# Kernel tuning notes

Measured on AMD Instinct MI355X. Metric: run time of the kernel, lower is better.

The kernel has to match this reference:

```python
import jax, jax.numpy as jnp
import numpy as np
from math import factorial as _f

# ---------- Wigner 3j / real Clebsch-Gordan (numpy, build-time) ----------

def _w3j(j1, j2, j3, m1, m2, m3):
    if m1 + m2 + m3 != 0 or not (abs(j1 - j2) <= j3 <= j1 + j2):
        return 0.0
    t1, t2 = j2 - m1 - j3, j1 + m2 - j3
    t3, t4, t5 = j1 + j2 - j3, j1 - m1, j2 + m2
    s = 0.0
    for t in range(max(0, t1, t2), min(t3, t4, t5) + 1):
        s += (-1.0) ** t / (_f(t) * _f(t - t1) * _f(t - t2) * _f(t3 - t) * _f(t4 - t) * _f(t5 - t))
    n = ((-1.0) ** (j1 - j2 - m3)
         * (_f(j1 + j2 - j3) * _f(j1 - j2 + j3) * _f(-j1 + j2 + j3) / _f(j1 + j2 + j3 + 1)) ** 0.5
         * (_f(j1 + m1) * _f(j1 - m1) * _f(j2 + m2) * _f(j2 - m2) * _f(j3 + m3) * _f(j3 - m3)) ** 0.5)
    return n * s


def _Umat(l):
    # complex -> real spherical-harmonic basis change
    U = np.zeros((2 * l + 1, 2 * l + 1), dtype=complex)
    U[l, l] = 1.0
    s2 = 1.0 / np.sqrt(2.0)
    for m in range(1, l + 1):
        U[l + m, l + m] = (-1.0) ** m * s2
        U[l + m, l - m] = s2
        U[l - m, l - m] = 1j * s2
        U[l - m, l + m] = -1j * (-1.0) ** m * s2
    return U


def _real_cg(l1, l2, l3):
    Cc = np.zeros((2 * l1 + 1, 2 * l2 + 1, 2 * l3 + 1), dtype=complex)
    for m1 in range(-l1, l1 + 1):
        for m2 in range(-l2, l2 + 1):
            m3 = m1 + m2
            if abs(m3) <= l3:
                Cc[l1 + m1, l2 + m2, l3 + m3] = ((-1.0) ** (l1 - l2 + m3) * np.sqrt(2 * l3 + 1)
                                                 * _w3j(l1, l2, l3, m1, m2, -m3))
    C = np.einsum('am,bn,co,mno->abc', _Umat(l1), _Umat(l2), np.conj(_Umat(l3)), Cc)
    C = C.imag if np.abs(C.imag).sum() > np.abs(C.real).sum() else C.real
    C = C / np.sqrt((C ** 2).sum())  # w3j normalization
    return (C * np.sqrt(2 * l3 + 1)).astype(np.float32)  # component normalization

_TRIPLES = [(1, 1, 2), (1, 2, 3), (0, 0, 0), (1, 1, 0), (2, 2, 0),
            (0, 1, 1), (1, 0, 1), (1, 2, 1), (2, 1, 1), (3, 2, 1),
            (0, 2, 2), (2, 0, 2), (2, 2, 2), (3, 1, 2)]
_CG = {k: jnp.asarray(_real_cg(*k)) for k in _TRIPLES}

# tensor-product channel lists: (l_Y, l_V) pairs producing each output l (filter 0e+1o+2e)
_P_L0 = [(0, 0), (1, 1), (2, 2)]
_P_L1 = [(0, 1), (1, 0), (1, 2), (2, 1), (3, 2)]
_P_L2 = [(0, 2), (1, 1), (2, 0), (2, 2), (3, 1)]
_EPS = 0.1       # epsilon (~1/sqrt(avg_num_neighbors))
_ENV_P = 6       # polynomial envelope order


def _sph(u):
    # component-normalized real spherical harmonics l=0..3 of unit vectors u, m=-l..l order
    E = u.shape[0]
    y0 = jnp.ones((E, 1), u.dtype)
    y1 = np.float32(np.sqrt(3.0)) * u[:, jnp.array([1, 2, 0])]  # real l=1 basis (y,z,x)
    t2 = jnp.einsum('abc,ea,eb->ec', _CG[(1, 1, 2)], y1, y1)
    y2 = t2 * (np.float32(np.sqrt(5.0)) / jnp.linalg.norm(t2, axis=-1, keepdims=True))
    t3 = jnp.einsum('abc,ea,eb->ec', _CG[(1, 2, 3)], y1, y2)
    y3 = t3 * (np.float32(np.sqrt(7.0)) / jnp.linalg.norm(t3, axis=-1, keepdims=True))
    return jnp.concatenate([y0, y1, y2, y3], axis=-1)  # (E,16)


def _lin(h, W):
    return h @ (W / np.float32(np.sqrt(W.shape[0])))  # fan-in normalized linear


def _envelope(d):
    p = _ENV_P
    c1 = np.float32((p + 1) * (p + 2) / 2.0)
    c2 = np.float32(p * (p + 2))
    c3 = np.float32(p * (p + 1) / 2.0)
    f = 1.0 - c1 * d ** p + c2 * d ** (p + 1) - c3 * d ** (p + 2)
    return jnp.where(d < 1.0, f, 0.0)


def _forward(vectors, x, V, senders, n_nodes, W1, W2a, W2b, W2c, Wv1, Wv2):
    E = vectors.shape[0]
    lengths = jnp.linalg.norm(vectors, axis=-1)            # (E,)
    Y = _sph(vectors / lengths[:, None])                   # (E,16)
    w = _lin(x, W1)                                        # (E,64) edge weights
    wY = w[:, :, None] * Y[:, None, :]                     # (E,64,16)
    node = jax.ops.segment_sum(wY, senders, num_segments=n_nodes)
    wY = node[senders] * np.float32(_EPS)                  # scatter_sum with map_back
    A = {0: wY[..., 0:1], 1: wY[..., 1:4], 2: wY[..., 4:9], 3: wY[..., 9:16]}
    B = {0: V[..., 0:1], 1: V[..., 1:4], 2: V[..., 4:9]}

    def tp(pairs, l3):
        outs = [jnp.einsum('abc,eua,eub->euc', _CG[(l1, l2, l3)], A[l1], B[l2])
                for (l1, l2) in pairs]
        return jnp.stack(outs, axis=2)                     # (E,64,n_pairs,2l3+1)

    S = tp(_P_L0, 0).reshape(E, -1)                        # (E,192) 0e scalars -> join x
    V1 = tp(_P_L1, 1).reshape(E, -1, 3)                    # (E,320,3) 1o
    V2 = tp(_P_L2, 2).reshape(E, -1, 5)                    # (E,320,5) 2e

    x2 = jnp.concatenate([x, S], axis=1)                   # (E, d_x+192)
    h = jax.nn.silu(_lin(x2, W2a))
    h = jax.nn.silu(_lin(h, W2b))
    h = _lin(h, W2c)                                       # (E,64), no output act
    x_out = _envelope(lengths)[:, None] * h                # smoothing envelope

    V1o = jnp.einsum('euc,uk->ekc', V1, Wv1 / np.float32(np.sqrt(Wv1.shape[0])))  # (E,64,3)
    V2e = jnp.einsum('euc,uk->ekc', V2, Wv2 / np.float32(np.sqrt(Wv2.shape[0])))  # (E,64,5)
    V_out = jnp.concatenate([V1o.reshape(E, -1), V2e.reshape(E, -1)], axis=1)     # (E,512)
    return x_out, V_out


def setup_inputs() -> dict:
    key = jax.random.key(0)
    ks = jax.random.split(key, 12)
    E, N, DX, MUL = 32768, 2048, 128, 64
    vectors = jax.random.uniform(ks[0], (E, 3), jnp.float32) - 0.5  # |r| < 1 (inside cutoff)
    x = jax.random.normal(ks[1], (E, DX), jnp.float32)
    V = jax.random.normal(ks[2], (E, MUL, 9), jnp.float32)          # 64 slots x (0e+1o+2e)
    senders = jax.random.randint(ks[3], (E,), 0, N)
    species = jax.random.randint(ks[4], (N,), 0, 4, jnp.int32)
    W1 = jax.random.normal(ks[5], (DX, MUL), jnp.float32)
    W2a = jax.random.normal(ks[6], (DX + 192, 64), jnp.float32)
    W2b = jax.random.normal(ks[7], (64, 64), jnp.float32)
    W2c = jax.random.normal(ks[8], (64, 64), jnp.float32)
    Wv1 = jax.random.normal(ks[9], (320, 64), jnp.float32)
    Wv2 = jax.random.normal(ks[10], (320, 64), jnp.float32)
    return dict(vectors=vectors, x=x, V=V, senders=senders, species=species,
                W1=W1, W2a=W2a, W2b=W2b, W2c=W2c, Wv1=Wv1, Wv2=Wv2)


def reference(vectors, x, V, senders, species, W1, W2a, W2b, W2c, Wv1, Wv2):
    # species is unused by the layer body (matches original signature)
    return _forward(vectors, x, V, senders, int(species.shape[0]), W1, W2a, W2b, W2c, Wv1, Wv2)
```

## Files before the change

kernel.cpp:

```cpp
#include <hip/hip_runtime.h>
#include <cmath>
#include <complex>
#include <vector>
#include <algorithm>

namespace {

static double factd(int n) { double r = 1; for (int i = 2; i <= n; i++) r *= i; return r; }
static double par(int k) { return (k % 2 == 0) ? 1.0 : -1.0; }

static double w3j(int j1, int j2, int j3, int m1, int m2, int m3) {
    if (m1 + m2 + m3 != 0) return 0.0;
    if (j3 < std::abs(j1 - j2) || j3 > j1 + j2) return 0.0;
    int t1 = j2 - m1 - j3, t2 = j1 + m2 - j3;
    int t3 = j1 + j2 - j3, t4 = j1 - m1, t5 = j2 + m2;
    int lo = std::max(0, std::max(t1, t2)), hi = std::min(t3, std::min(t4, t5));
    double s = 0.0;
    for (int t = lo; t <= hi; t++)
        s += par(t) / (factd(t) * factd(t - t1) * factd(t - t2) *
                       factd(t3 - t) * factd(t4 - t) * factd(t5 - t));
    double n = par(j1 - j2 - m3)
        * std::sqrt(factd(j1 + j2 - j3) * factd(j1 - j2 + j3) * factd(-j1 + j2 + j3) / factd(j1 + j2 + j3 + 1))
        * std::sqrt(factd(j1 + m1) * factd(j1 - m1) * factd(j2 + m2) * factd(j2 - m2) * factd(j3 + m3) * factd(j3 - m3));
    return n * s;
}

static void Umat(int l, std::complex<double>* U) {
    int n = 2 * l + 1;
    for (int i = 0; i < n * n; i++) U[i] = 0.0;
    U[l * n + l] = 1.0;
    double s2 = 1.0 / std::sqrt(2.0);
    for (int m = 1; m <= l; m++) {
        U[(l + m) * n + (l + m)] = par(m) * s2;
        U[(l + m) * n + (l - m)] = s2;
        U[(l - m) * n + (l - m)] = std::complex<double>(0.0, s2);
        U[(l - m) * n + (l + m)] = std::complex<double>(0.0, -par(m) * s2);
    }
}

static void real_cg(int l1, int l2, int l3, float* out) {
    int n1 = 2 * l1 + 1, n2 = 2 * l2 + 1, n3 = 2 * l3 + 1;
    std::vector<std::complex<double>> Cc((size_t)n1 * n2 * n3, 0.0);
    for (int m1 = -l1; m1 <= l1; m1++)
        for (int m2 = -l2; m2 <= l2; m2++) {
            int m3 = m1 + m2;
            if (std::abs(m3) <= l3)
                Cc[((size_t)(l1 + m1) * n2 + (l2 + m2)) * n3 + (l3 + m3)] =
                    par(l1 - l2 + m3) * std::sqrt((double)(2 * l3 + 1)) * w3j(l1, l2, l3, m1, m2, -m3);
        }
    std::vector<std::complex<double>> U1((size_t)n1 * n1), U2((size_t)n2 * n2), U3((size_t)n3 * n3);
    Umat(l1, U1.data()); Umat(l2, U2.data()); Umat(l3, U3.data());
    std::vector<std::complex<double>> C((size_t)n1 * n2 * n3, 0.0);
    for (int a = 0; a < n1; a++)
        for (int b = 0; b < n2; b++)
            for (int c = 0; c < n3; c++) {
                std::complex<double> s = 0.0;
                for (int m = 0; m < n1; m++)
                    for (int nn = 0; nn < n2; nn++) {
                        std::complex<double> u12 = U1[(size_t)a * n1 + m] * U2[(size_t)b * n2 + nn];
                        if (u12 == std::complex<double>(0.0, 0.0)) continue;
                        for (int o = 0; o < n3; o++) {
                            std::complex<double> cc = Cc[((size_t)m * n2 + nn) * n3 + o];
                            if (cc == std::complex<double>(0.0, 0.0)) continue;
                            s += u12 * std::conj(U3[(size_t)c * n3 + o]) * cc;
                        }
                    }
                C[((size_t)a * n2 + b) * n3 + c] = s;
            }
    double sim = 0, sre = 0;
    for (auto& z : C) { sim += std::abs(z.imag()); sre += std::abs(z.real()); }
    std::vector<double> R(C.size());
    for (size_t i = 0; i < C.size(); i++) R[i] = (sim > sre) ? C[i].imag() : C[i].real();
    double ss = 0; for (double v : R) ss += v * v;
    double scale = std::sqrt((double)(2 * l3 + 1)) / std::sqrt(ss);
    for (size_t i = 0; i < R.size(); i++) out[i] = (float)(R[i] * scale);
}

}

struct CGPack {
    float c000[1];  float c110[9];   float c220[25];
    float c011[9];  float c101[9];   float c121[45];  float c211[45]; float c321[105];
    float c022[25]; float c202[25];  float c222[125]; float c312[105];
    float c112[45]; float c123[105];
};

static void build_pack(CGPack& p) {
    real_cg(0, 0, 0, p.c000); real_cg(1, 1, 0, p.c110); real_cg(2, 2, 0, p.c220);
    real_cg(0, 1, 1, p.c011); real_cg(1, 0, 1, p.c101); real_cg(1, 2, 1, p.c121);
    real_cg(2, 1, 1, p.c211); real_cg(3, 2, 1, p.c321);
    real_cg(0, 2, 2, p.c022); real_cg(2, 0, 2, p.c202); real_cg(2, 2, 2, p.c222);
    real_cg(3, 1, 2, p.c312); real_cg(1, 1, 2, p.c112); real_cg(1, 2, 3, p.c123);
}


template <int NA, int NB, int NC>
__device__ __forceinline__ void tpc(const float* __restrict__ C,
                                    const float* __restrict__ a,
                                    const float* __restrict__ b,
                                    float* __restrict__ out) {
#pragma unroll
    for (int c = 0; c < NC; c++) {
        float s = 0.f;
#pragma unroll
        for (int i = 0; i < NA; i++) {
#pragma unroll
            for (int j = 0; j < NB; j++)
                s += C[(i * NB + j) * NC + c] * a[i] * b[j];
        }
        out[c] = s;
    }
}

template <int NA, int NB, int NC, int ST>
__device__ __forceinline__ void tpcs(const float* __restrict__ C,
                                     const float* __restrict__ a,
                                     const float* __restrict__ b,
                                     float* __restrict__ out) {
#pragma unroll
    for (int c = 0; c < NC; c++) {
        float s = 0.f;
#pragma unroll
        for (int i = 0; i < NA; i++) {
#pragma unroll
            for (int j = 0; j < NB; j++)
                s += C[(i * NB + j) * NC + c] * a[i] * b[j];
        }
        out[c * ST] = s;
    }
}

__device__ __forceinline__ float silu(float v) { return v / (1.f + expf(-v)); }

#define EPSC 0.1f
#define INV_SQRT128 0.08838834764831845f
#define INV_SQRT320 0.05590169943749474f
#define SQRT5 2.2360679774997896f
#define SQRT7 2.6457513110645907f
#define SQRT3 1.7320508075688772f

__global__ __launch_bounds__(256) void k_fuse_wv(
    const float* __restrict__ Wv1, const float* __restrict__ Wv2,
    float2* __restrict__ WvI) {
    int i = blockIdx.x * blockDim.x + threadIdx.x;
    if (i < 320 * 64) WvI[i] = make_float2(Wv1[i], Wv2[i]);
}

__global__ __launch_bounds__(256) void k_edge_pre(
    const float* __restrict__ vectors, const float* __restrict__ x,
    const int* __restrict__ senders, const float* __restrict__ W1,
    float* __restrict__ node, int E, CGPack cg) {
    int wid = (blockIdx.x * blockDim.x + threadIdx.x) >> 6;
    int lane = threadIdx.x & 63;
    if (wid >= E) return;
    int e = wid;
    float vx = vectors[e * 3 + 0], vy = vectors[e * 3 + 1], vz = vectors[e * 3 + 2];
    float inv = rsqrtf(vx * vx + vy * vy + vz * vz);
    float ux = vx * inv, uy = vy * inv, uz = vz * inv;

    float Y[16];
    Y[0] = 1.f;
    float y1[3] = { SQRT3 * uy, SQRT3 * uz, SQRT3 * ux };
    float t2[5]; tpc<3, 3, 5>(cg.c112, y1, y1, t2);
    float n2 = 0.f;
#pragma unroll
    for (int c = 0; c < 5; c++) n2 += t2[c] * t2[c];
    float sc2 = SQRT5 * rsqrtf(n2);
    float y2[5];
#pragma unroll
    for (int c = 0; c < 5; c++) y2[c] = t2[c] * sc2;
    float t3[7]; tpc<3, 5, 7>(cg.c123, y1, y2, t3);
    float n3 = 0.f;
#pragma unroll
    for (int c = 0; c < 7; c++) n3 += t3[c] * t3[c];
    float sc3 = SQRT7 * rsqrtf(n3);
#pragma unroll
    for (int j = 0; j < 3; j++) Y[1 + j] = y1[j];
#pragma unroll
    for (int j = 0; j < 5; j++) Y[4 + j] = y2[j];
#pragma unroll
    for (int j = 0; j < 7; j++) Y[9 + j] = t3[j] * sc3;

    const float* xr = x + (size_t)e * 128;
    float w = 0.f;
#pragma unroll 4
    for (int d = 0; d < 128; d++) w += xr[d] * W1[d * 64 + lane];
    w *= INV_SQRT128;

    int s = senders[e];
    float* nb = node + (size_t)s * 1024 + lane;
#pragma unroll
    for (int k = 0; k < 16; k++) atomicAdd(nb + k * 64, w * Y[k]);
}

__global__ __launch_bounds__(64, 4) void k_edge_main(
    const float* __restrict__ vectors, const float* __restrict__ x,
    const float* __restrict__ V, const int* __restrict__ senders,
    const float* __restrict__ node, const float2* __restrict__ WvI,
    const float* __restrict__ W2a, const float* __restrict__ W2b, const float* __restrict__ W2c,
    float* __restrict__ xout, float* __restrict__ vout, int E, CGPack cg) {
    __shared__ __align__(16) float V1sh[3][320];
    __shared__ __align__(16) float V2sh[5][320];
    __shared__ float Ssh[192];
    __shared__ float Hsh[64];

    int e = blockIdx.x;
    int u = threadIdx.x;
    int s = senders[e];

    const float* nb = node + (size_t)s * 1024 + u;
    float a0 = nb[0] * EPSC;
    float a1[3], a2[5], a3[7];
#pragma unroll
    for (int j = 0; j < 3; j++) a1[j] = nb[(1 + j) * 64] * EPSC;
#pragma unroll
    for (int j = 0; j < 5; j++) a2[j] = nb[(4 + j) * 64] * EPSC;
#pragma unroll
    for (int j = 0; j < 7; j++) a3[j] = nb[(9 + j) * 64] * EPSC;

    const float* vb = V + (size_t)e * 576 + u * 9;
    float b0 = vb[0];
    float b1[3] = { vb[1], vb[2], vb[3] };
    float b2[5] = { vb[4], vb[5], vb[6], vb[7], vb[8] };

    {
        float o[1];
        Ssh[u * 3 + 0] = cg.c000[0] * a0 * b0;
        tpc<3, 3, 1>(cg.c110, a1, b1, o); Ssh[u * 3 + 1] = o[0];
        tpc<5, 5, 1>(cg.c220, a2, b2, o); Ssh[u * 3 + 2] = o[0];
    }
    {
        float* v1 = &V1sh[0][u * 5];
        tpcs<1, 3, 3, 320>(cg.c011, &a0, b1, v1 + 0);
        tpcs<3, 1, 3, 320>(cg.c101, a1, &b0, v1 + 1);
        tpcs<3, 5, 3, 320>(cg.c121, a1, b2, v1 + 2);
        tpcs<5, 3, 3, 320>(cg.c211, a2, b1, v1 + 3);
        tpcs<7, 5, 3, 320>(cg.c321, a3, b2, v1 + 4);
    }
    {
        float* v2 = &V2sh[0][u * 5];
        tpcs<1, 5, 5, 320>(cg.c022, &a0, b2, v2 + 0);
        tpcs<3, 3, 5, 320>(cg.c112, a1, b1, v2 + 1);
        tpcs<5, 1, 5, 320>(cg.c202, a2, &b0, v2 + 2);
        tpcs<5, 5, 5, 320>(cg.c222, a2, b2, v2 + 3);
        tpcs<7, 3, 5, 320>(cg.c312, a3, b1, v2 + 4);
    }
    __syncthreads();

    const float* xr = x + (size_t)e * 128;
    float h = 0.f;
    for (int d = 0; d < 128; d++) h += xr[d] * W2a[d * 64 + u];
    for (int j = 0; j < 192; j++) h += Ssh[j] * W2a[(128 + j) * 64 + u];
    h = silu(h * INV_SQRT320);
    Hsh[u] = h;
    __syncthreads();
    float h2 = 0.f;
    for (int j = 0; j < 64; j++) h2 += Hsh[j] * W2b[j * 64 + u];
    h2 = silu(h2 * 0.125f);
    __syncthreads();
    Hsh[u] = h2;
    __syncthreads();
    float h3 = 0.f;
    for (int j = 0; j < 64; j++) h3 += Hsh[j] * W2c[j * 64 + u];
    h3 *= 0.125f;

    float vx = vectors[e * 3 + 0], vy = vectors[e * 3 + 1], vz = vectors[e * 3 + 2];
    float len = sqrtf(vx * vx + vy * vy + vz * vz);
    float d2 = len * len, d4 = d2 * d2, d6 = d4 * d2, d7 = d6 * len, d8 = d7 * len;
    float env = 1.f - 28.f * d6 + 48.f * d7 - 21.f * d8;
    if (!(len < 1.f)) env = 0.f;
    xout[(size_t)e * 64 + u] = env * h3;

    float acc1[3] = { 0.f, 0.f, 0.f };
    float acc2[5] = { 0.f, 0.f, 0.f, 0.f, 0.f };
    const float2* wvp = WvI + u;
    for (int t4 = 0; t4 < 80; ++t4) {
        int t = t4 * 4;
        float2 w0 = wvp[(t + 0) * 64];
        float2 w1 = wvp[(t + 1) * 64];
        float2 w2 = wvp[(t + 2) * 64];
        float2 w3 = wvp[(t + 3) * 64];
#pragma unroll
        for (int c = 0; c < 3; c++) {
            float4 v = *(const float4*)&V1sh[c][t];
            acc1[c] += v.x * w0.x + v.y * w1.x + v.z * w2.x + v.w * w3.x;
        }
#pragma unroll
        for (int c = 0; c < 5; c++) {
            float4 v = *(const float4*)&V2sh[c][t];
            acc2[c] += v.x * w0.y + v.y * w1.y + v.z * w2.y + v.w * w3.y;
        }
    }
    float* vo = vout + (size_t)e * 512;
#pragma unroll
    for (int c = 0; c < 3; c++) vo[u * 3 + c] = acc1[c] * INV_SQRT320;
#pragma unroll
    for (int c = 0; c < 5; c++) vo[192 + u * 5 + c] = acc2[c] * INV_SQRT320;
}

extern "C" void kernel_launch(void* const* d_in, const int* in_sizes, int n_in,
                              void* d_out, int out_size, void* d_ws, size_t ws_size,
                              hipStream_t stream) {
    const float* vectors = (const float*)d_in[0];
    const float* x       = (const float*)d_in[1];
    const float* V       = (const float*)d_in[2];
    const int*   senders = (const int*)d_in[3];
    const float* W1  = (const float*)d_in[5];
    const float* W2a = (const float*)d_in[6];
    const float* W2b = (const float*)d_in[7];
    const float* W2c = (const float*)d_in[8];
    const float* Wv1 = (const float*)d_in[9];
    const float* Wv2 = (const float*)d_in[10];

    int E = in_sizes[0] / 3;
    int N = in_sizes[4];

    CGPack pack;
    build_pack(pack);

    float*  node = (float*)d_ws;
    float2* WvI  = (float2*)((char*)d_ws + (size_t)N * 1024 * sizeof(float));
    hipMemsetAsync(node, 0, (size_t)N * 1024 * sizeof(float), stream);

    hipLaunchKernelGGL(k_fuse_wv, dim3((320 * 64 + 255) / 256), dim3(256), 0, stream,
                       Wv1, Wv2, WvI);

    dim3 blkA(256), grdA((unsigned)(((size_t)E * 64 + 255) / 256));
    hipLaunchKernelGGL(k_edge_pre, grdA, blkA, 0, stream,
                       vectors, x, senders, W1, node, E, pack);

    float* xout = (float*)d_out;
    float* vout = xout + (size_t)E * 64;
    hipLaunchKernelGGL(k_edge_main, dim3((unsigned)E), dim3(64), 0, stream,
                       vectors, x, V, senders, node, WvI,
                       W2a, W2b, W2c, xout, vout, E, pack);
}
```

Baseline: 747.9 us.

## Repack weights into float4 interleaved layout and make node features lane-contiguous

```diff
diff --git a/kernel.cpp b/kernel.cpp
--- a/kernel.cpp
+++ b/kernel.cpp
@@ -131,6 +131,9 @@
 }
 
 __device__ __forceinline__ float silu(float v) { return v / (1.f + expf(-v)); }
+__device__ __forceinline__ float dot4(float4 a, float4 b) {
+    return a.x * b.x + a.y * b.y + a.z * b.z + a.w * b.w;
+}
 
 #define EPSC 0.1f
 #define INV_SQRT128 0.08838834764831845f
@@ -139,16 +142,45 @@
 #define SQRT7 2.6457513110645907f
 #define SQRT3 1.7320508075688772f
 
-__global__ __launch_bounds__(256) void k_fuse_wv(
+#define N_WVQ  (160 * 64)
+#define N_W2A  (80 * 64)
+#define N_W2B  (16 * 64)
+#define N_W2C  (16 * 64)
+#define N_W1I  (32 * 64)
+
+__global__ __launch_bounds__(256) void k_pack(
     const float* __restrict__ Wv1, const float* __restrict__ Wv2,
-    float2* __restrict__ WvI) {
+    const float* __restrict__ W2a, const float* __restrict__ W2b, const float* __restrict__ W2c,
+    const float* __restrict__ W1,
+    float4* __restrict__ WvQ, float4* __restrict__ W2aI,
+    float4* __restrict__ W2bI, float4* __restrict__ W2cI, float4* __restrict__ W1I) {
     int i = blockIdx.x * blockDim.x + threadIdx.x;
-    if (i < 320 * 64) WvI[i] = make_float2(Wv1[i], Wv2[i]);
+    if (i < N_WVQ) {
+        int t2 = i >> 6, u = i & 63;
+        WvQ[i] = make_float4(Wv1[(2 * t2) * 64 + u], Wv2[(2 * t2) * 64 + u],
+                             Wv1[(2 * t2 + 1) * 64 + u], Wv2[(2 * t2 + 1) * 64 + u]);
+    } else if (i < N_WVQ + N_W2A) {
+        int j = i - N_WVQ; int g = j >> 6, u = j & 63;
+        W2aI[j] = make_float4(W2a[(4 * g) * 64 + u], W2a[(4 * g + 1) * 64 + u],
+                              W2a[(4 * g + 2) * 64 + u], W2a[(4 * g + 3) * 64 + u]);
+    } else if (i < N_WVQ + N_W2A + N_W2B) {
+        int j = i - N_WVQ - N_W2A; int g = j >> 6, u = j & 63;
+        W2bI[j] = make_float4(W2b[(4 * g) * 64 + u], W2b[(4 * g + 1) * 64 + u],
+                              W2b[(4 * g + 2) * 64 + u], W2b[(4 * g + 3) * 64 + u]);
+    } else if (i < N_WVQ + N_W2A + N_W2B + N_W2C) {
+        int j = i - N_WVQ - N_W2A - N_W2B; int g = j >> 6, u = j & 63;
+        W2cI[j] = make_float4(W2c[(4 * g) * 64 + u], W2c[(4 * g + 1) * 64 + u],
+                              W2c[(4 * g + 2) * 64 + u], W2c[(4 * g + 3) * 64 + u]);
+    } else if (i < N_WVQ + N_W2A + N_W2B + N_W2C + N_W1I) {
+        int j = i - N_WVQ - N_W2A - N_W2B - N_W2C; int g = j >> 6, u = j & 63;
+        W1I[j] = make_float4(W1[(4 * g) * 64 + u], W1[(4 * g + 1) * 64 + u],
+                             W1[(4 * g + 2) * 64 + u], W1[(4 * g + 3) * 64 + u]);
+    }
 }
 
 __global__ __launch_bounds__(256) void k_edge_pre(
     const float* __restrict__ vectors, const float* __restrict__ x,
-    const int* __restrict__ senders, const float* __restrict__ W1,
+    const int* __restrict__ senders, const float4* __restrict__ W1I,
     float* __restrict__ node, int E, CGPack cg) {
     int wid = (blockIdx.x * blockDim.x + threadIdx.x) >> 6;
     int lane = threadIdx.x & 63;
@@ -181,42 +213,40 @@
 #pragma unroll
     for (int j = 0; j < 7; j++) Y[9 + j] = t3[j] * sc3;
 
-    const float* xr = x + (size_t)e * 128;
+    const float4* xr4 = (const float4*)(x + (size_t)e * 128);
     float w = 0.f;
-#pragma unroll 4
-    for (int d = 0; d < 128; d++) w += xr[d] * W1[d * 64 + lane];
+#pragma unroll 8
+    for (int g = 0; g < 32; g++) w += dot4(xr4[g], W1I[g * 64 + lane]);
     w *= INV_SQRT128;
 
     int s = senders[e];
-    float* nb = node + (size_t)s * 1024 + lane;
-#pragma unroll
-    for (int k = 0; k < 16; k++) atomicAdd(nb + k * 64, w * Y[k]);
+    float* nb = node + (size_t)s * 1024 + lane * 16;
+#pragma unroll
+    for (int k = 0; k < 16; k++) atomicAdd(nb + k, w * Y[k]);
 }
 
 __global__ __launch_bounds__(64, 4) void k_edge_main(
     const float* __restrict__ vectors, const float* __restrict__ x,
     const float* __restrict__ V, const int* __restrict__ senders,
-    const float* __restrict__ node, const float2* __restrict__ WvI,
-    const float* __restrict__ W2a, const float* __restrict__ W2b, const float* __restrict__ W2c,
+    const float* __restrict__ node, const float4* __restrict__ WvQ,
+    const float4* __restrict__ W2aI, const float4* __restrict__ W2bI, const float4* __restrict__ W2cI,
     float* __restrict__ xout, float* __restrict__ vout, int E, CGPack cg) {
     __shared__ __align__(16) float V1sh[3][320];
     __shared__ __align__(16) float V2sh[5][320];
-    __shared__ float Ssh[192];
-    __shared__ float Hsh[64];
+    __shared__ __align__(16) float Ssh[192];
+    __shared__ __align__(16) float Hsh[64];
 
     int e = blockIdx.x;
     int u = threadIdx.x;
     int s = senders[e];
 
-    const float* nb = node + (size_t)s * 1024 + u;
-    float a0 = nb[0] * EPSC;
-    float a1[3], a2[5], a3[7];
-#pragma unroll
-    for (int j = 0; j < 3; j++) a1[j] = nb[(1 + j) * 64] * EPSC;
-#pragma unroll
-    for (int j = 0; j < 5; j++) a2[j] = nb[(4 + j) * 64] * EPSC;
-#pragma unroll
-    for (int j = 0; j < 7; j++) a3[j] = nb[(9 + j) * 64] * EPSC;
+    const float4* nb4 = (const float4*)(node + (size_t)s * 1024 + u * 16);
+    float4 g0 = nb4[0], g1 = nb4[1], g2 = nb4[2], g3 = nb4[3];
+    float a0 = g0.x * EPSC;
+    float a1[3] = { g0.y * EPSC, g0.z * EPSC, g0.w * EPSC };
+    float a2[5] = { g1.x * EPSC, g1.y * EPSC, g1.z * EPSC, g1.w * EPSC, g2.x * EPSC };
+    float a3[7] = { g2.y * EPSC, g2.z * EPSC, g2.w * EPSC, g3.x * EPSC,
+                    g3.y * EPSC, g3.z * EPSC, g3.w * EPSC };
 
     const float* vb = V + (size_t)e * 576 + u * 9;
     float b0 = vb[0];
@@ -247,21 +277,27 @@
     }
     __syncthreads();
 
-    const float* xr = x + (size_t)e * 128;
+    const float4* xr4 = (const float4*)(x + (size_t)e * 128);
     float h = 0.f;
-    for (int d = 0; d < 128; d++) h += xr[d] * W2a[d * 64 + u];
-    for (int j = 0; j < 192; j++) h += Ssh[j] * W2a[(128 + j) * 64 + u];
+#pragma unroll 8
+    for (int g = 0; g < 32; g++) h += dot4(xr4[g], W2aI[g * 64 + u]);
+    const float4* S4 = (const float4*)Ssh;
+#pragma unroll 8
+    for (int g = 0; g < 48; g++) h += dot4(S4[g], W2aI[(32 + g) * 64 + u]);
     h = silu(h * INV_SQRT320);
     Hsh[u] = h;
     __syncthreads();
+    const float4* H4 = (const float4*)Hsh;
     float h2 = 0.f;
-    for (int j = 0; j < 64; j++) h2 += Hsh[j] * W2b[j * 64 + u];
+#pragma unroll 8
+    for (int g = 0; g < 16; g++) h2 += dot4(H4[g], W2bI[g * 64 + u]);
     h2 = silu(h2 * 0.125f);
     __syncthreads();
     Hsh[u] = h2;
     __syncthreads();
     float h3 = 0.f;
-    for (int j = 0; j < 64; j++) h3 += Hsh[j] * W2c[j * 64 + u];
+#pragma unroll 8
+    for (int g = 0; g < 16; g++) h3 += dot4(H4[g], W2cI[g * 64 + u]);
     h3 *= 0.125f;
 
     float vx = vectors[e * 3 + 0], vy = vectors[e * 3 + 1], vz = vectors[e * 3 + 2];
@@ -273,22 +309,20 @@
 
     float acc1[3] = { 0.f, 0.f, 0.f };
     float acc2[5] = { 0.f, 0.f, 0.f, 0.f, 0.f };
-    const float2* wvp = WvI + u;
+    const float4* wvp = WvQ + u;
     for (int t4 = 0; t4 < 80; ++t4) {
+        float4 wq0 = wvp[(2 * t4) * 64];
+        float4 wq1 = wvp[(2 * t4 + 1) * 64];
         int t = t4 * 4;
-        float2 w0 = wvp[(t + 0) * 64];
-        float2 w1 = wvp[(t + 1) * 64];
-        float2 w2 = wvp[(t + 2) * 64];
-        float2 w3 = wvp[(t + 3) * 64];
 #pragma unroll
         for (int c = 0; c < 3; c++) {
             float4 v = *(const float4*)&V1sh[c][t];
-            acc1[c] += v.x * w0.x + v.y * w1.x + v.z * w2.x + v.w * w3.x;
+            acc1[c] += v.x * wq0.x + v.y * wq0.z + v.z * wq1.x + v.w * wq1.z;
         }
 #pragma unroll
         for (int c = 0; c < 5; c++) {
             float4 v = *(const float4*)&V2sh[c][t];
-            acc2[c] += v.x * w0.y + v.y * w1.y + v.z * w2.y + v.w * w3.y;
+            acc2[c] += v.x * wq0.y + v.y * wq0.w + v.z * wq1.y + v.w * wq1.w;
         }
     }
     float* vo = vout + (size_t)e * 512;
@@ -318,20 +352,27 @@
     CGPack pack;
     build_pack(pack);
 
-    float*  node = (float*)d_ws;
-    float2* WvI  = (float2*)((char*)d_ws + (size_t)N * 1024 * sizeof(float));
+    char* wp = (char*)d_ws;
+    float*  node = (float*)wp;                 wp += (size_t)N * 1024 * sizeof(float);
+    float4* WvQ  = (float4*)wp;                wp += (size_t)N_WVQ * sizeof(float4);
+    float4* W2aI = (float4*)wp;                wp += (size_t)N_W2A * sizeof(float4);
+    float4* W2bI = (float4*)wp;                wp += (size_t)N_W2B * sizeof(float4);
+    float4* W2cI = (float4*)wp;                wp += (size_t)N_W2C * sizeof(float4);
+    float4* W1I  = (float4*)wp;                wp += (size_t)N_W1I * sizeof(float4);
+
     hipMemsetAsync(node, 0, (size_t)N * 1024 * sizeof(float), stream);
 
-    hipLaunchKernelGGL(k_fuse_wv, dim3((320 * 64 + 255) / 256), dim3(256), 0, stream,
-                       Wv1, Wv2, WvI);
+    int npack = N_WVQ + N_W2A + N_W2B + N_W2C + N_W1I;
+    hipLaunchKernelGGL(k_pack, dim3((npack + 255) / 256), dim3(256), 0, stream,
+                       Wv1, Wv2, W2a, W2b, W2c, W1, WvQ, W2aI, W2bI, W2cI, W1I);
 
     dim3 blkA(256), grdA((unsigned)(((size_t)E * 64 + 255) / 256));
     hipLaunchKernelGGL(k_edge_pre, grdA, blkA, 0, stream,
-                       vectors, x, senders, W1, node, E, pack);
+                       vectors, x, senders, W1I, node, E, pack);
 
     float* xout = (float*)d_out;
     float* vout = xout + (size_t)E * 64;
     hipLaunchKernelGGL(k_edge_main, dim3((unsigned)E), dim3(64), 0, stream,
-                       vectors, x, V, senders, node, WvI,
-                       W2a, W2b, W2c, xout, vout, E, pack);
-}
+                       vectors, x, V, senders, node, WvQ,
+                       W2aI, W2bI, W2cI, xout, vout, E, pack);
+}
```

New measurement: 2.291 ms. 206% more time.
